# Kernel optimization log

Measured on AMD Instinct MI355X. Metric: run time of the kernel, lower is better.

## Reference

```python
import jax, jax.numpy as jnp
from jax import lax
import numpy as np

NEG = -1e9  # -inf surrogate for DP boundaries (matches deepblast's large-negative init)


def _lstm(xe, W_ih, W_hh, b):
    # xe: (B, T, D) -> hidden states (B, T, H). Single-layer LSTM via lax.scan.
    B, T, _ = xe.shape
    H = W_hh.shape[0]
    pre = xe @ W_ih + b  # precompute input contributions: (B, T, 4H)
    def step(carry, p):
        h, c = carry
        z = p + h @ W_hh
        i, f, g, o = jnp.split(z, 4, axis=-1)
        c = jax.nn.sigmoid(f) * c + jax.nn.sigmoid(i) * jnp.tanh(g)
        h = jax.nn.sigmoid(o) * jnp.tanh(c)
        return (h, c), h
    h0 = jnp.zeros((B, H), xe.dtype)
    _, hs = lax.scan(step, (h0, h0), jnp.swapaxes(pre, 0, 1))
    return jnp.swapaxes(hs, 0, 1)


def _embed(tok, emb, W_ih, W_hh, b_lstm, W_out, b_out):
    # StackedRNN: token embedding -> LSTM -> linear projection to nembed
    return _lstm(emb[tok], W_ih, W_hh, b_lstm) @ W_out + b_out


def _nw(theta, A):
    # Softmax-relaxed Needleman-Wunsch terminal value, anti-diagonal wavefront scan.
    # V[i,j] = theta[i-1,j-1] + logsumexp(V[i-1,j-1], V[i-1,j]+A, V[i,j-1]+A)
    B, N, M = theta.shape
    ii = jnp.arange(N + 1)
    d0 = jnp.full((B, N + 1), NEG, theta.dtype).at[:, 0].set(0.0)  # diag k=0: V[0,0]=0
    d1 = jnp.full((B, N + 1), NEG, theta.dtype)                    # diag k=1: boundaries
    def shift(a):  # a[i] -> a[i-1]
        return jnp.concatenate([jnp.full((a.shape[0], 1), NEG, a.dtype), a[:, :-1]], axis=1)
    def step(carry, k):
        p2, p1 = carry  # diagonals k-2, k-1; entry i holds V[i, (k-2)-i] / V[i, (k-1)-i]
        jj = k - ii
        valid = (ii >= 1) & (ii <= N) & (jj >= 1) & (jj <= M)
        td = theta[:, jnp.clip(ii - 1, 0, N - 1), jnp.clip(jj - 1, 0, M - 1)]  # (B, N+1)
        v = jax.nn.logsumexp(jnp.stack([shift(p1) + A, shift(p2), p1 + A], 0), axis=0)
        cur = jnp.where(valid[None, :], td + v, NEG)
        return (p1, cur), None
    (_, last), _ = lax.scan(step, (d0, d1), jnp.arange(2, N + M + 1))
    return last[:, N]  # V[N, M] per batch


def setup_inputs() -> dict:
    key = jax.random.key(0)
    ks = jax.random.split(key, 10)
    B, T, V, E, H = 32, 512, 22, 512, 512
    return {
        "x": jax.random.randint(ks[0], (B, T), 0, V),
        "y": jax.random.randint(ks[1], (B, T), 0, V),
        "emb": jax.random.normal(ks[2], (V, E), jnp.float32) * 0.1,
        "W_ih": jax.random.normal(ks[3], (E, 4 * H), jnp.float32) * 0.05,
        "W_hh": jax.random.normal(ks[4], (H, 4 * H), jnp.float32) * 0.05,
        "b_lstm": jnp.zeros((4 * H,), jnp.float32),
        "W_out": jax.random.normal(ks[5], (H, E), jnp.float32) * 0.05,
        "b_out": jnp.zeros((E,), jnp.float32),
        "W_gap": jax.random.normal(ks[6], (2 * E, 1), jnp.float32) * 0.05,
        "b_gap": jnp.zeros((1,), jnp.float32),
    }


def reference(x, y, emb, W_ih, W_hh, b_lstm, W_out, b_out, W_gap, b_gap):
    zx = _embed(x, emb, W_ih, W_hh, b_lstm, W_out, b_out)  # (B, N, E)
    zy = _embed(y, emb, W_ih, W_hh, b_lstm, W_out, b_out)  # (B, M, E)
    theta = jnp.einsum('bid,bjd->bij', zx, zy)             # (B, N, M)
    merged = jnp.concatenate([zx.mean(1), zy.mean(1)], axis=1)
    A = merged @ W_gap + b_gap                             # (B, 1) learned gap score
    return _nw(theta, A)                                   # (B,) DP terminal value
```

## Files before the change

kernel.cpp:

```cpp
#include <hip/hip_runtime.h>
#include <math.h>

#define TSEQ 512
#define HDIM 512
#define EDIM 512
#define NB   32
#define ROWS 64
#define GATES 2048
#define NEGV -1000000000.0f

typedef __attribute__((ext_vector_type(8))) short bf16x8;
typedef __attribute__((ext_vector_type(4))) float f32x4;

__device__ __forceinline__ float sigf(float x){ return 1.0f/(1.0f + __expf(-x)); }

__device__ __forceinline__ float tanhfast(float x){
  float t = __expf(-2.0f*fabsf(x));
  float r = (1.0f - t)/(1.0f + t);
  return copysignf(r, x);
}

__device__ __forceinline__ unsigned short f2bf(float f){
  unsigned int u = __builtin_bit_cast(unsigned int, f);
  unsigned int r = (u + 0x7fff + ((u>>16)&1)) >> 16;
  return (unsigned short)r;
}

__global__ __launch_bounds__(256) void table_k(const float* __restrict__ emb,
        const float* __restrict__ W_ih, const float* __restrict__ b_lstm,
        float* __restrict__ table){
  int j = blockIdx.x*256 + threadIdx.x;
  int v = blockIdx.y;
  float acc = b_lstm[j];
  #pragma unroll 4
  for(int k=0;k<EDIM;k++) acc = fmaf(emb[v*EDIM+k], W_ih[(size_t)k*GATES+j], acc);
  table[(size_t)v*GATES+j] = acc;
}

__global__ __launch_bounds__(64) void wprep_k(const float* __restrict__ W_hh,
        unsigned short* __restrict__ Wswz){
  int cid = blockIdx.x;
  int lane = threadIdx.x;
  int js = cid>>6, g = (cid>>4)&3, kc = cid&15;
  int col = g*512 + js*16 + (lane&15);
  int kbase = kc*32 + (lane>>4)*8;
  unsigned short v[8];
  #pragma unroll
  for(int e=0;e<8;e++) v[e] = f2bf(W_hh[(size_t)(kbase+e)*GATES + col]);
  *(uint4*)&Wswz[((size_t)cid*64 + lane)*8] = *(const uint4*)v;
}

__global__ __launch_bounds__(64) void wprep2_k(const float* __restrict__ W_out,
        unsigned short* __restrict__ wsw){
  int cid = blockIdx.x;
  int lane = threadIdx.x;
  int nc = cid>>4, kc = cid&15;
  int col = nc*16 + (lane&15);
  int kb = kc*32 + (lane>>4)*8;
  unsigned short v[8];
  #pragma unroll
  for(int e=0;e<8;e++) v[e] = f2bf(W_out[(size_t)(kb+e)*EDIM + col]);
  *(uint4*)&wsw[((size_t)cid*64 + lane)*8] = *(const uint4*)v;
}

__global__ __launch_bounds__(64,1) void lstm_wave(const int* __restrict__ x, const int* __restrict__ y,
        const float* __restrict__ table, const unsigned short* __restrict__ Wswz,
        unsigned* __restrict__ hx, unsigned short* __restrict__ hsb){
  __shared__ unsigned short wlds[32768];
  int w = blockIdx.x;
  int c = w>>6, mh = (w>>5)&1, js = w&31;
  int gid = w>>5;
  int lane = threadIdx.x;

  {
    const uint4* src = (const uint4*)(Wswz + (size_t)js*32768);
    uint4* dst = (uint4*)wlds;
    #pragma unroll
    for(int i=0;i<64;i++) dst[lane + i*64] = src[lane + i*64];
  }
  __syncthreads();

  const int* tokbase = c ? y : x;
  int jloc = lane&15;
  int j    = js*16 + jloc;
  int hi   = (j>>3)&3;
  int kc_o = j>>5;
  int e_o  = j&7;
  int rl0  = (lane>>4)*4;
  unsigned pub_vo = (unsigned)(((kc_o*64 + (rl0|(hi<<4)))*8 + e_o)*4);
  int rbase = c*32 + mh*16 + rl0;
  float cst[4] = {0.f,0.f,0.f,0.f};

  unsigned* gbase = hx + (size_t)gid*16384;
  unsigned vo32 = (unsigned)lane*32u;

  for(int s=0;s<TSEQ;s++){
    const unsigned* hin = gbase + (size_t)(s&1)*8192;
    unsigned* hout      = gbase + (size_t)((s+1)&1)*8192;
    unsigned tagexp = (unsigned)s;

    uint4 ra[32];
    while(true){
      #pragma unroll
      for(int kc=0;kc<16;kc++){
        asm volatile(
          "global_load_dwordx4 %0, %2, %3 sc0 sc1\n\t"
          "global_load_dwordx4 %1, %2, %3 offset:16 sc0 sc1"
          : "=&v"(ra[2*kc]), "=&v"(ra[2*kc+1])
          : "v"(vo32), "s"((const void*)(hin + (size_t)kc*512))
          : "memory");
      }
      asm volatile("s_waitcnt vmcnt(0)" ::: "memory");
      __builtin_amdgcn_sched_barrier(0);
      unsigned acc = 0u;
      #pragma unroll
      for(int i=0;i<32;i++)
        acc |= (ra[i].x ^ tagexp) | (ra[i].y ^ tagexp) | (ra[i].z ^ tagexp) | (ra[i].w ^ tagexp);
      if(__all((int)((acc & 0xFFFFu) == 0u))) break;
    }

    bf16x8 af[16];
    #pragma unroll
    for(int kc=0;kc<16;kc++){
      uint4 pk_;
      pk_.x = (ra[2*kc].x  >>16) | (ra[2*kc].y  & 0xFFFF0000u);
      pk_.y = (ra[2*kc].z  >>16) | (ra[2*kc].w  & 0xFFFF0000u);
      pk_.z = (ra[2*kc+1].x>>16) | (ra[2*kc+1].y& 0xFFFF0000u);
      pk_.w = (ra[2*kc+1].z>>16) | (ra[2*kc+1].w& 0xFFFF0000u);
      af[kc] = __builtin_bit_cast(bf16x8, pk_);
    }

    f32x4 acc0={0,0,0,0}, acc1={0,0,0,0}, acc2={0,0,0,0}, acc3={0,0,0,0};
    #pragma unroll
    for(int kc=0;kc<16;kc++){
      bf16x8 w0 = *(const bf16x8*)(const void*)&wlds[((0*16+kc)*64 + lane)*8];
      bf16x8 w1 = *(const bf16x8*)(const void*)&wlds[((1*16+kc)*64 + lane)*8];
      bf16x8 w2 = *(const bf16x8*)(const void*)&wlds[((2*16+kc)*64 + lane)*8];
      bf16x8 w3 = *(const bf16x8*)(const void*)&wlds[((3*16+kc)*64 + lane)*8];
      acc0 = __builtin_amdgcn_mfma_f32_16x16x32_bf16(af[kc], w0, acc0, 0,0,0);
      acc1 = __builtin_amdgcn_mfma_f32_16x16x32_bf16(af[kc], w1, acc1, 0,0,0);
      acc2 = __builtin_amdgcn_mfma_f32_16x16x32_bf16(af[kc], w2, acc2, 0,0,0);
      acc3 = __builtin_amdgcn_mfma_f32_16x16x32_bf16(af[kc], w3, acc3, 0,0,0);
    }

    unsigned hv[4]; unsigned short hb16[4];
    int sc = s>>4, sl = s&15;
    unsigned tagw = (unsigned)(s+1);
    #pragma unroll
    for(int q=0;q<4;q++){
      int tok = tokbase[(mh*16 + rl0 + q)*TSEQ + s];
      const float* tbl = table + (size_t)tok*GATES;
      float zi = acc0[q] + tbl[j];
      float zf = acc1[q] + tbl[512+j];
      float zg = acc2[q] + tbl[1024+j];
      float zo = acc3[q] + tbl[1536+j];
      float cn = sigf(zf)*cst[q] + sigf(zi)*tanhfast(zg);
      float h  = sigf(zo)*tanhfast(cn);
      cst[q] = cn;
      unsigned short hbv = f2bf(h);
      hb16[q] = hbv;
      hv[q] = ((unsigned)hbv<<16) | tagw;
    }
    asm volatile(
      "global_store_dword %[a], %[d0], %[sb] sc0 sc1\n\t"
      "global_store_dword %[a], %[d1], %[sb] offset:32 sc0 sc1\n\t"
      "global_store_dword %[a], %[d2], %[sb] offset:64 sc0 sc1\n\t"
      "global_store_dword %[a], %[d3], %[sb] offset:96 sc0 sc1"
      :: [a]"v"(pub_vo), [d0]"v"(hv[0]),[d1]"v"(hv[1]),[d2]"v"(hv[2]),[d3]"v"(hv[3]),
         [sb]"s"((void*)hout)
      : "memory");
    #pragma unroll
    for(int q=0;q<4;q++){
      int r = rbase + q;
      int mc = r*32 + sc;
      hsb[((size_t)(mc*16 + kc_o)*64 + (sl|(hi<<4)))*8 + e_o] = hb16[q];
    }
  }
}

__global__ __launch_bounds__(256) void zproj_mfma(const unsigned short* __restrict__ hsb,
        const unsigned short* __restrict__ woutswz, const float* __restrict__ b_out,
        float* __restrict__ z, unsigned short* __restrict__ zxA, unsigned short* __restrict__ zyB){
  int tid = threadIdx.x, wv = tid>>6, lane = tid&63;
  int m0 = blockIdx.x*128 + (wv>>1)*64;
  int n0 = blockIdx.y*128 + (wv&1)*64;
  int mc0 = m0>>4, nc0 = n0>>4;
  const uint4* ha = (const uint4*)hsb;
  const uint4* wb = (const uint4*)woutswz;
  f32x4 acc[4][4];
  #pragma unroll
  for(int i=0;i<4;i++)
    #pragma unroll
    for(int k2=0;k2<4;k2++) acc[i][k2] = (f32x4){0,0,0,0};
  for(int kc=0;kc<16;kc++){
    bf16x8 a[4], b[4];
    #pragma unroll
    for(int i=0;i<4;i++){
      a[i] = __builtin_bit_cast(bf16x8, ha[((size_t)((mc0+i)*16 + kc))*64 + lane]);
      b[i] = __builtin_bit_cast(bf16x8, wb[((size_t)((nc0+i)*16 + kc))*64 + lane]);
    }
    #pragma unroll
    for(int mi=0;mi<4;mi++)
      #pragma unroll
      for(int ci=0;ci<4;ci++)
        acc[mi][ci] = __builtin_amdgcn_mfma_f32_16x16x32_bf16(a[mi], b[ci], acc[mi][ci], 0,0,0);
  }
  int r = m0>>9;
  bool isx = (r < NB);
  unsigned short* zb = isx ? zxA : zyB;
  int bb = isx ? r : r-NB;
  #pragma unroll
  for(int ci=0;ci<4;ci++){
    int n = n0 + ci*16 + (lane&15);
    float bo = b_out[n];
    int kcz = n>>5, hi = (n>>3)&3, ez = n&7;
    #pragma unroll
    for(int mi=0;mi<4;mi++){
      #pragma unroll
      for(int q=0;q<4;q++){
        int m = m0 + mi*16 + (lane>>4)*4 + q;
        float zv = acc[mi][ci][q] + bo;
        z[(size_t)m*EDIM + n] = zv;
        int i = m&511;
        zb[(((size_t)(bb*32 + (i>>4))*16 + kcz)*64 + ((i&15)|(hi<<4)))*8 + ez] = f2bf(zv);
      }
    }
  }
}

__global__ __launch_bounds__(256) void theta_mfma(const unsigned short* __restrict__ zxA,
        const unsigned short* __restrict__ zyB, float* __restrict__ thetaD){
  int tid = threadIdx.x, wv = tid>>6, lane = tid&63;
  int b = blockIdx.z;
  int i0 = blockIdx.x*128 + (wv>>1)*64;
  int j0 = blockIdx.y*128 + (wv&1)*64;
  int ic0 = i0>>4, jc0 = j0>>4;
  const uint4* pa = (const uint4*)zxA;
  const uint4* pb = (const uint4*)zyB;
  f32x4 acc[4][4];
  #pragma unroll
  for(int i=0;i<4;i++)
    #pragma unroll
    for(int k2=0;k2<4;k2++) acc[i][k2] = (f32x4){0,0,0,0};
  for(int kc=0;kc<16;kc++){
    bf16x8 a[4], bfr[4];
    #pragma unroll
    for(int i=0;i<4;i++){
      a[i]   = __builtin_bit_cast(bf16x8, pa[((size_t)(b*32 + ic0+i)*16 + kc)*64 + lane]);
      bfr[i] = __builtin_bit_cast(bf16x8, pb[((size_t)(b*32 + jc0+i)*16 + kc)*64 + lane]);
    }
    #pragma unroll
    for(int mi=0;mi<4;mi++)
      #pragma unroll
      for(int ci=0;ci<4;ci++)
        acc[mi][ci] = __builtin_amdgcn_mfma_f32_16x16x32_bf16(a[mi], bfr[ci], acc[mi][ci], 0,0,0);
  }
  #pragma unroll
  for(int mi=0;mi<4;mi++){
    #pragma unroll
    for(int ci=0;ci<4;ci++){
      #pragma unroll
      for(int q=0;q<4;q++){
        int i  = i0 + mi*16 + (lane>>4)*4 + q;
        int jj = j0 + ci*16 + (lane&15);
        thetaD[((size_t)b*1023 + (i+jj))*512 + i] = acc[mi][ci][q];
      }
    }
  }
}

__global__ __launch_bounds__(256) void mean_k(const float* __restrict__ z, float* __restrict__ zmean){
  int r = blockIdx.x;
  int tid = threadIdx.x;
  for(int ee=tid; ee<EDIM; ee+=256){
    float acc=0.f;
    for(int t=0;t<TSEQ;t++) acc += z[((size_t)r*TSEQ+t)*EDIM+ee];
    zmean[(size_t)r*EDIM+ee] = acc*(1.0f/TSEQ);
  }
}

__global__ __launch_bounds__(256) void gap_k(const float* __restrict__ zmean,
        const float* __restrict__ W_gap, const float* __restrict__ b_gap, float* __restrict__ Aout){
  __shared__ float red[256];
  int b = blockIdx.x;
  int tid = threadIdx.x;
  float acc=0.f;
  for(int i=tid;i<2*EDIM;i+=256){
    float m = (i<EDIM)? zmean[(size_t)b*EDIM+i] : zmean[(size_t)(b+NB)*EDIM + (i-EDIM)];
    acc = fmaf(m, W_gap[i], acc);
  }
  red[tid]=acc; __syncthreads();
  for(int s=128;s>0;s>>=1){ if(tid<s) red[tid]+=red[tid+s]; __syncthreads(); }
  if(tid==0) Aout[b] = red[0] + b_gap[0];
}

__global__ __launch_bounds__(64) void nw_k(const float* __restrict__ thetaD,
        const float* __restrict__ Aout, float* __restrict__ out){
  const float L2E = 1.4426950408889634f, LN2 = 0.6931471805599453f;
  int b = blockIdx.x;
  int lane = threadIdx.x;
  float A = Aout[b];
  const float* thD = thetaD + (size_t)b*1023*512;
  float p1[8], p2[8];
  #pragma unroll
  for(int i=0;i<8;i++){ p1[i]=NEGV; p2[i]=NEGV; }
  float p1_0 = NEGV, p2_0 = 0.0f;
  float4 ta = *(const float4*)&thD[(size_t)lane*8];
  float4 tb = *(const float4*)&thD[(size_t)lane*8+4];
  for(int k=2;k<=1024;k++){
    float4 na, nb;
    if(k<1024){
      na = *(const float4*)&thD[(size_t)(k-1)*512 + lane*8];
      nb = *(const float4*)&thD[(size_t)(k-1)*512 + lane*8+4];
    }
    float pm1 = __shfl_up(p1[7],1);
    float pm2 = __shfl_up(p2[7],1);
    if(lane==0){ pm1 = p1_0; pm2 = p2_0; }
    float td[8] = {ta.x,ta.y,ta.z,ta.w,tb.x,tb.y,tb.z,tb.w};
    float cur[8];
    #pragma unroll
    for(int cx=0;cx<8;cx++){
      int i = lane*8+1+cx;
      int jq = k-i;
      bool valid = (jq>=1)&&(jq<=512);
      float a  = (cx==0? pm1 : p1[cx-1]) + A;
      float bb = (cx==0? pm2 : p2[cx-1]);
      float cc = p1[cx] + A;
      float m = fmaxf(fmaxf(a,bb),cc);
      float sum = exp2f((a-m)*L2E) + exp2f((bb-m)*L2E) + exp2f((cc-m)*L2E);
      float v = m + log2f(sum)*LN2;
      cur[cx] = valid ? td[cx] + v : NEGV;
    }
    #pragma unroll
    for(int cx=0;cx<8;cx++){ p2[cx]=p1[cx]; p1[cx]=cur[cx]; }
    p2_0 = p1_0; p1_0 = NEGV;
    ta = na; tb = nb;
  }
  if(lane==63) out[b] = p1[7];
}

extern "C" void kernel_launch(void* const* d_in, const int* in_sizes, int n_in,
                              void* d_out, int out_size, void* d_ws, size_t ws_size,
                              hipStream_t stream) {
  (void)in_sizes; (void)n_in; (void)out_size; (void)ws_size;
  const int*   x      = (const int*)d_in[0];
  const int*   y      = (const int*)d_in[1];
  const float* emb    = (const float*)d_in[2];
  const float* W_ih   = (const float*)d_in[3];
  const float* W_hh   = (const float*)d_in[4];
  const float* b_lstm = (const float*)d_in[5];
  const float* W_out  = (const float*)d_in[6];
  const float* b_out  = (const float*)d_in[7];
  const float* W_gap  = (const float*)d_in[8];
  const float* b_gap  = (const float*)d_in[9];
  float* out = (float*)d_out;

  char* ws = (char*)d_ws;
  const size_t OFF_TABLE = 0;
  const size_t OFF_WSWZ  = 184320;
  const size_t OFF_WOUT  = OFF_WSWZ  + 2097152;
  const size_t OFF_HX    = OFF_WOUT  + 524288;
  const size_t OFF_HSB   = OFF_HX    + 262144;
  const size_t OFF_Z     = OFF_HSB   + 33554432;
  const size_t OFF_ZXA   = OFF_Z     + 67108864;
  const size_t OFF_ZYB   = OFF_ZXA   + 16777216;
  const size_t OFF_THD   = OFF_ZYB   + 16777216;
  const size_t OFF_ZMEAN = OFF_THD   + 67043328;
  const size_t OFF_AOUT  = OFF_ZMEAN + 131072;
  float* table = (float*)(ws + OFF_TABLE);
  unsigned short* Wswz    = (unsigned short*)(ws + OFF_WSWZ);
  unsigned short* woutswz = (unsigned short*)(ws + OFF_WOUT);
  unsigned* hx = (unsigned*)(ws + OFF_HX);
  unsigned short* hsb = (unsigned short*)(ws + OFF_HSB);
  float* z     = (float*)(ws + OFF_Z);
  unsigned short* zxA = (unsigned short*)(ws + OFF_ZXA);
  unsigned short* zyB = (unsigned short*)(ws + OFF_ZYB);
  float* thetaD = (float*)(ws + OFF_THD);
  float* zmean = (float*)(ws + OFF_ZMEAN);
  float* Aout  = (float*)(ws + OFF_AOUT);

  hipMemsetAsync(hx, 0, 262144, stream);

  table_k<<<dim3(8,22), 256, 0, stream>>>(emb, W_ih, b_lstm, table);
  wprep_k<<<2048, 64, 0, stream>>>(W_hh, Wswz);
  wprep2_k<<<512, 64, 0, stream>>>(W_out, woutswz);
  lstm_wave<<<128, 64, 0, stream>>>(x, y, table, Wswz, hx, hsb);
  zproj_mfma<<<dim3(256,4), 256, 0, stream>>>(hsb, woutswz, b_out, z, zxA, zyB);
  theta_mfma<<<dim3(4,4,32), 256, 0, stream>>>(zxA, zyB, thetaD);
  mean_k<<<64, 256, 0, stream>>>(z, zmean);
  gap_k<<<32, 256, 0, stream>>>(zmean, W_gap, b_gap, Aout);
  nw_k<<<32, 64, 0, stream>>>(thetaD, Aout, out);
}
```

Before: 3.013 ms.

## Register-resident LSTM weights, fused mean, bf16 theta with tiled diagonal transpose

Several changes at once. The LSTM kernel keeps three of the four gate weight slices in registers and only the fourth in LDS, prefetches the token table values before the spin-wait, adds s_sleep to the poll loop, and swaps divisions for rcp. The projection kernel stops writing the full fp32 z and instead accumulates column sums into zmean with atomics, which removes the mean kernel. Theta is stored in bf16 row-major and a new LDS-tiled kernel reorders it to anti-diagonal layout, replacing the earlier scattered writes; the NW kernel reads bf16. This cuts memory traffic and per-step latency, at the cost of bf16 precision in theta, heavy register pressure, and possibly extra latency from the sleep.

```diff
diff --git a/kernel.cpp b/kernel.cpp
--- a/kernel.cpp
+++ b/kernel.cpp
@@ -12,11 +12,11 @@
 typedef __attribute__((ext_vector_type(8))) short bf16x8;
 typedef __attribute__((ext_vector_type(4))) float f32x4;
 
-__device__ __forceinline__ float sigf(float x){ return 1.0f/(1.0f + __expf(-x)); }
+__device__ __forceinline__ float sigf(float x){ return __builtin_amdgcn_rcpf(1.0f + __expf(-x)); }
 
 __device__ __forceinline__ float tanhfast(float x){
   float t = __expf(-2.0f*fabsf(x));
-  float r = (1.0f - t)/(1.0f + t);
+  float r = (1.0f - t)*__builtin_amdgcn_rcpf(1.0f + t);
   return copysignf(r, x);
 }
 
@@ -24,6 +24,11 @@
   unsigned int u = __builtin_bit_cast(unsigned int, f);
   unsigned int r = (u + 0x7fff + ((u>>16)&1)) >> 16;
   return (unsigned short)r;
+}
+
+__device__ __forceinline__ float bf2f(unsigned short v){
+  unsigned int u = ((unsigned int)v)<<16;
+  return __builtin_bit_cast(float, u);
 }
 
 __global__ __launch_bounds__(256) void table_k(const float* __restrict__ emb,
@@ -66,17 +71,26 @@
 __global__ __launch_bounds__(64,1) void lstm_wave(const int* __restrict__ x, const int* __restrict__ y,
         const float* __restrict__ table, const unsigned short* __restrict__ Wswz,
         unsigned* __restrict__ hx, unsigned short* __restrict__ hsb){
-  __shared__ unsigned short wlds[32768];
+  __shared__ unsigned short wlds[8192];
   int w = blockIdx.x;
   int c = w>>6, mh = (w>>5)&1, js = w&31;
-  int gid = w>>5;
+  int gid = c*2 + mh;
   int lane = threadIdx.x;
 
+  bf16x8 wf[48];
   {
-    const uint4* src = (const uint4*)(Wswz + (size_t)js*32768);
+    const unsigned short* wp = Wswz + (size_t)js*32768;
+    #pragma unroll
+    for(int g=0;g<3;g++)
+      #pragma unroll
+      for(int kc=0;kc<16;kc++)
+        wf[g*16+kc] = *(const bf16x8*)(const void*)&wp[((size_t)(g*16+kc)*64 + lane)*8];
+  }
+  {
+    const uint4* src = (const uint4*)(Wswz + (size_t)js*32768 + 48*512);
     uint4* dst = (uint4*)wlds;
     #pragma unroll
-    for(int i=0;i<64;i++) dst[lane + i*64] = src[lane + i*64];
+    for(int i=0;i<16;i++) dst[lane + i*64] = src[lane + i*64];
   }
   __syncthreads();
 
@@ -99,7 +113,20 @@
     unsigned* hout      = gbase + (size_t)((s+1)&1)*8192;
     unsigned tagexp = (unsigned)s;
 
+    float tb[4][4];
+    {
+      int toks[4];
+      #pragma unroll
+      for(int q=0;q<4;q++) toks[q] = tokbase[(mh*16 + rl0 + q)*TSEQ + s];
+      #pragma unroll
+      for(int q=0;q<4;q++){
+        const float* tbl = table + (size_t)toks[q]*GATES;
+        tb[0][q]=tbl[j]; tb[1][q]=tbl[512+j]; tb[2][q]=tbl[1024+j]; tb[3][q]=tbl[1536+j];
+      }
+    }
+
     uint4 ra[32];
+    int att = 0;
     while(true){
       #pragma unroll
       for(int kc=0;kc<16;kc++){
@@ -117,9 +144,11 @@
       for(int i=0;i<32;i++)
         acc |= (ra[i].x ^ tagexp) | (ra[i].y ^ tagexp) | (ra[i].z ^ tagexp) | (ra[i].w ^ tagexp);
       if(__all((int)((acc & 0xFFFFu) == 0u))) break;
-    }
-
-    bf16x8 af[16];
+      __builtin_amdgcn_s_sleep(2);
+      att++;
+    }
+
+    f32x4 acc0={0,0,0,0}, acc1={0,0,0,0}, acc2={0,0,0,0}, acc3={0,0,0,0};
     #pragma unroll
     for(int kc=0;kc<16;kc++){
       uint4 pk_;
@@ -127,20 +156,12 @@
       pk_.y = (ra[2*kc].z  >>16) | (ra[2*kc].w  & 0xFFFF0000u);
       pk_.z = (ra[2*kc+1].x>>16) | (ra[2*kc+1].y& 0xFFFF0000u);
       pk_.w = (ra[2*kc+1].z>>16) | (ra[2*kc+1].w& 0xFFFF0000u);
-      af[kc] = __builtin_bit_cast(bf16x8, pk_);
-    }
-
-    f32x4 acc0={0,0,0,0}, acc1={0,0,0,0}, acc2={0,0,0,0}, acc3={0,0,0,0};
-    #pragma unroll
-    for(int kc=0;kc<16;kc++){
-      bf16x8 w0 = *(const bf16x8*)(const void*)&wlds[((0*16+kc)*64 + lane)*8];
-      bf16x8 w1 = *(const bf16x8*)(const void*)&wlds[((1*16+kc)*64 + lane)*8];
-      bf16x8 w2 = *(const bf16x8*)(const void*)&wlds[((2*16+kc)*64 + lane)*8];
-      bf16x8 w3 = *(const bf16x8*)(const void*)&wlds[((3*16+kc)*64 + lane)*8];
-      acc0 = __builtin_amdgcn_mfma_f32_16x16x32_bf16(af[kc], w0, acc0, 0,0,0);
-      acc1 = __builtin_amdgcn_mfma_f32_16x16x32_bf16(af[kc], w1, acc1, 0,0,0);
-      acc2 = __builtin_amdgcn_mfma_f32_16x16x32_bf16(af[kc], w2, acc2, 0,0,0);
-      acc3 = __builtin_amdgcn_mfma_f32_16x16x32_bf16(af[kc], w3, acc3, 0,0,0);
+      bf16x8 afk = __builtin_bit_cast(bf16x8, pk_);
+      acc0 = __builtin_amdgcn_mfma_f32_16x16x32_bf16(afk, wf[kc],    acc0, 0,0,0);
+      acc1 = __builtin_amdgcn_mfma_f32_16x16x32_bf16(afk, wf[16+kc], acc1, 0,0,0);
+      acc2 = __builtin_amdgcn_mfma_f32_16x16x32_bf16(afk, wf[32+kc], acc2, 0,0,0);
+      bf16x8 b3 = *(const bf16x8*)(const void*)&wlds[((size_t)kc*64 + lane)*8];
+      acc3 = __builtin_amdgcn_mfma_f32_16x16x32_bf16(afk, b3,        acc3, 0,0,0);
     }
 
     unsigned hv[4]; unsigned short hb16[4];
@@ -148,12 +169,10 @@
     unsigned tagw = (unsigned)(s+1);
     #pragma unroll
     for(int q=0;q<4;q++){
-      int tok = tokbase[(mh*16 + rl0 + q)*TSEQ + s];
-      const float* tbl = table + (size_t)tok*GATES;
-      float zi = acc0[q] + tbl[j];
-      float zf = acc1[q] + tbl[512+j];
-      float zg = acc2[q] + tbl[1024+j];
-      float zo = acc3[q] + tbl[1536+j];
+      float zi = acc0[q] + tb[0][q];
+      float zf = acc1[q] + tb[1][q];
+      float zg = acc2[q] + tb[2][q];
+      float zo = acc3[q] + tb[3][q];
       float cn = sigf(zf)*cst[q] + sigf(zi)*tanhfast(zg);
       float h  = sigf(zo)*tanhfast(cn);
       cst[q] = cn;
@@ -180,7 +199,8 @@
 
 __global__ __launch_bounds__(256) void zproj_mfma(const unsigned short* __restrict__ hsb,
         const unsigned short* __restrict__ woutswz, const float* __restrict__ b_out,
-        float* __restrict__ z, unsigned short* __restrict__ zxA, unsigned short* __restrict__ zyB){
+        unsigned short* __restrict__ zxA, unsigned short* __restrict__ zyB,
+        float* __restrict__ zmean){
   int tid = threadIdx.x, wv = tid>>6, lane = tid&63;
   int m0 = blockIdx.x*128 + (wv>>1)*64;
   int n0 = blockIdx.y*128 + (wv&1)*64;
@@ -214,22 +234,26 @@
     int n = n0 + ci*16 + (lane&15);
     float bo = b_out[n];
     int kcz = n>>5, hi = (n>>3)&3, ez = n&7;
+    float colsum = 0.f;
     #pragma unroll
     for(int mi=0;mi<4;mi++){
       #pragma unroll
       for(int q=0;q<4;q++){
         int m = m0 + mi*16 + (lane>>4)*4 + q;
         float zv = acc[mi][ci][q] + bo;
-        z[(size_t)m*EDIM + n] = zv;
+        colsum += acc[mi][ci][q];
         int i = m&511;
         zb[(((size_t)(bb*32 + (i>>4))*16 + kcz)*64 + ((i&15)|(hi<<4)))*8 + ez] = f2bf(zv);
       }
     }
+    colsum += __shfl_xor(colsum, 16);
+    colsum += __shfl_xor(colsum, 32);
+    if((lane>>4)==0) atomicAdd(&zmean[(size_t)r*EDIM + n], colsum);
   }
 }
 
 __global__ __launch_bounds__(256) void theta_mfma(const unsigned short* __restrict__ zxA,
-        const unsigned short* __restrict__ zyB, float* __restrict__ thetaD){
+        const unsigned short* __restrict__ zyB, unsigned short* __restrict__ th_n){
   int tid = threadIdx.x, wv = tid>>6, lane = tid&63;
   int b = blockIdx.z;
   int i0 = blockIdx.x*128 + (wv>>1)*64;
@@ -263,30 +287,53 @@
       for(int q=0;q<4;q++){
         int i  = i0 + mi*16 + (lane>>4)*4 + q;
         int jj = j0 + ci*16 + (lane&15);
-        thetaD[((size_t)b*1023 + (i+jj))*512 + i] = acc[mi][ci][q];
+        th_n[((size_t)b*TSEQ + i)*TSEQ + jj] = f2bf(acc[mi][ci][q]);
       }
     }
   }
 }
 
-__global__ __launch_bounds__(256) void mean_k(const float* __restrict__ z, float* __restrict__ zmean){
-  int r = blockIdx.x;
+#define DP 136
+__global__ __launch_bounds__(128) void diag_k(const unsigned short* __restrict__ th_n,
+        unsigned short* __restrict__ thD){
+  __shared__ unsigned short t[128*DP];
+  int b = blockIdx.z;
+  int i0 = blockIdx.x*128;
+  int j0 = blockIdx.y*128;
   int tid = threadIdx.x;
-  for(int ee=tid; ee<EDIM; ee+=256){
-    float acc=0.f;
-    for(int t=0;t<TSEQ;t++) acc += z[((size_t)r*TSEQ+t)*EDIM+ee];
-    zmean[(size_t)r*EDIM+ee] = acc*(1.0f/TSEQ);
+  {
+    int cc = (tid&7)*16;
+    for(int rr = tid>>3; rr<128; rr+=16){
+      const uint4* src = (const uint4*)&th_n[((size_t)(b*TSEQ + i0+rr))*TSEQ + j0 + cc];
+      uint4 v0 = src[0], v1 = src[1];
+      *(uint4*)&t[rr*DP + cc]     = v0;
+      *(uint4*)&t[rr*DP + cc + 8] = v1;
+    }
+  }
+  __syncthreads();
+  for(int u=0;u<255;u++){
+    int d = i0 + j0 + u;
+    int ibeg = (u>127) ? (d - j0 - 127) : i0;
+    int iend = (u<128) ? (d - j0)       : (i0+127);
+    int len = iend - ibeg + 1;
+    if(tid < len){
+      int i = ibeg + tid;
+      thD[((size_t)b*1023 + d)*TSEQ + i] = t[(i-i0)*DP + (d-i-j0)];
+    }
   }
 }
 
 __global__ __launch_bounds__(256) void gap_k(const float* __restrict__ zmean,
-        const float* __restrict__ W_gap, const float* __restrict__ b_gap, float* __restrict__ Aout){
+        const float* __restrict__ b_out, const float* __restrict__ W_gap,
+        const float* __restrict__ b_gap, float* __restrict__ Aout){
   __shared__ float red[256];
   int b = blockIdx.x;
   int tid = threadIdx.x;
   float acc=0.f;
   for(int i=tid;i<2*EDIM;i+=256){
-    float m = (i<EDIM)? zmean[(size_t)b*EDIM+i] : zmean[(size_t)(b+NB)*EDIM + (i-EDIM)];
+    int e = (i<EDIM)? i : i-EDIM;
+    float msum = (i<EDIM)? zmean[(size_t)b*EDIM+e] : zmean[(size_t)(b+NB)*EDIM+e];
+    float m = msum*(1.0f/TSEQ) + b_out[e];
     acc = fmaf(m, W_gap[i], acc);
   }
   red[tid]=acc; __syncthreads();
@@ -294,29 +341,29 @@
   if(tid==0) Aout[b] = red[0] + b_gap[0];
 }
 
-__global__ __launch_bounds__(64) void nw_k(const float* __restrict__ thetaD,
+__global__ __launch_bounds__(64) void nw_k(const unsigned short* __restrict__ thD,
         const float* __restrict__ Aout, float* __restrict__ out){
   const float L2E = 1.4426950408889634f, LN2 = 0.6931471805599453f;
   int b = blockIdx.x;
   int lane = threadIdx.x;
   float A = Aout[b];
-  const float* thD = thetaD + (size_t)b*1023*512;
+  const unsigned short* thb = thD + (size_t)b*1023*TSEQ;
   float p1[8], p2[8];
   #pragma unroll
   for(int i=0;i<8;i++){ p1[i]=NEGV; p2[i]=NEGV; }
   float p1_0 = NEGV, p2_0 = 0.0f;
-  float4 ta = *(const float4*)&thD[(size_t)lane*8];
-  float4 tb = *(const float4*)&thD[(size_t)lane*8+4];
+  uint4 ta = *(const uint4*)&thb[(size_t)lane*8];
   for(int k=2;k<=1024;k++){
-    float4 na, nb;
-    if(k<1024){
-      na = *(const float4*)&thD[(size_t)(k-1)*512 + lane*8];
-      nb = *(const float4*)&thD[(size_t)(k-1)*512 + lane*8+4];
-    }
+    uint4 na = ta;
+    if(k<1024) na = *(const uint4*)&thb[(size_t)(k-1)*TSEQ + lane*8];
+    float td[8];
+    td[0]=bf2f((unsigned short)(ta.x&0xFFFF)); td[1]=bf2f((unsigned short)(ta.x>>16));
+    td[2]=bf2f((unsigned short)(ta.y&0xFFFF)); td[3]=bf2f((unsigned short)(ta.y>>16));
+    td[4]=bf2f((unsigned short)(ta.z&0xFFFF)); td[5]=bf2f((unsigned short)(ta.z>>16));
+    td[6]=bf2f((unsigned short)(ta.w&0xFFFF)); td[7]=bf2f((unsigned short)(ta.w>>16));
     float pm1 = __shfl_up(p1[7],1);
     float pm2 = __shfl_up(p2[7],1);
     if(lane==0){ pm1 = p1_0; pm2 = p2_0; }
-    float td[8] = {ta.x,ta.y,ta.z,ta.w,tb.x,tb.y,tb.z,tb.w};
     float cur[8];
     #pragma unroll
     for(int cx=0;cx<8;cx++){
@@ -334,7 +381,7 @@
     #pragma unroll
     for(int cx=0;cx<8;cx++){ p2[cx]=p1[cx]; p1[cx]=cur[cx]; }
     p2_0 = p1_0; p1_0 = NEGV;
-    ta = na; tb = nb;
+    ta = na;
   }
   if(lane==63) out[b] = p1[7];
 }
@@ -361,33 +408,34 @@
   const size_t OFF_WOUT  = OFF_WSWZ  + 2097152;
   const size_t OFF_HX    = OFF_WOUT  + 524288;
   const size_t OFF_HSB   = OFF_HX    + 262144;
-  const size_t OFF_Z     = OFF_HSB   + 33554432;
-  const size_t OFF_ZXA   = OFF_Z     + 67108864;
+  const size_t OFF_ZXA   = OFF_HSB   + 33554432;
   const size_t OFF_ZYB   = OFF_ZXA   + 16777216;
-  const size_t OFF_THD   = OFF_ZYB   + 16777216;
-  const size_t OFF_ZMEAN = OFF_THD   + 67043328;
+  const size_t OFF_THN   = OFF_ZYB   + 16777216;
+  const size_t OFF_THD   = OFF_THN   + 33554432;
+  const size_t OFF_ZMEAN = OFF_THD   + 33521664;
   const size_t OFF_AOUT  = OFF_ZMEAN + 131072;
   float* table = (float*)(ws + OFF_TABLE);
   unsigned short* Wswz    = (unsigned short*)(ws + OFF_WSWZ);
   unsigned short* woutswz = (unsigned short*)(ws + OFF_WOUT);
   unsigned* hx = (unsigned*)(ws + OFF_HX);
-  unsigned short* hsb = (unsigned short*)(ws + OFF_HSB);
-  float* z     = (float*)(ws + OFF_Z);
-  unsigned short* zxA = (unsigned short*)(ws + OFF_ZXA);
-  unsigned short* zyB = (unsigned short*)(ws + OFF_ZYB);
-  float* thetaD = (float*)(ws + OFF_THD);
+  unsigned short* hsb  = (unsigned short*)(ws + OFF_HSB);
+  unsigned short* zxA  = (unsigned short*)(ws + OFF_ZXA);
+  unsigned short* zyB  = (unsigned short*)(ws + OFF_ZYB);
+  unsigned short* th_n = (unsigned short*)(ws + OFF_THN);
+  unsigned short* thD  = (unsigned short*)(ws + OFF_THD);
   float* zmean = (float*)(ws + OFF_ZMEAN);
   float* Aout  = (float*)(ws + OFF_AOUT);
 
   hipMemsetAsync(hx, 0, 262144, stream);
+  hipMemsetAsync(zmean, 0, 131072, stream);
 
   table_k<<<dim3(8,22), 256, 0, stream>>>(emb, W_ih, b_lstm, table);
   wprep_k<<<2048, 64, 0, stream>>>(W_hh, Wswz);
   wprep2_k<<<512, 64, 0, stream>>>(W_out, woutswz);
   lstm_wave<<<128, 64, 0, stream>>>(x, y, table, Wswz, hx, hsb);
-  zproj_mfma<<<dim3(256,4), 256, 0, stream>>>(hsb, woutswz, b_out, z, zxA, zyB);
-  theta_mfma<<<dim3(4,4,32), 256, 0, stream>>>(zxA, zyB, thetaD);
-  mean_k<<<64, 256, 0, stream>>>(z, zmean);
-  gap_k<<<32, 256, 0, stream>>>(zmean, W_gap, b_gap, Aout);
-  nw_k<<<32, 64, 0, stream>>>(thetaD, Aout, out);
-}
+  zproj_mfma<<<dim3(256,4), 256, 0, stream>>>(hsb, woutswz, b_out, zxA, zyB, zmean);
+  theta_mfma<<<dim3(4,4,32), 256, 0, stream>>>(zxA, zyB, th_n);
+  diag_k<<<dim3(4,4,32), 128, 0, stream>>>(th_n, thD);
+  gap_k<<<32, 256, 0, stream>>>(zmean, b_out, W_gap, b_gap, Aout);
+  nw_k<<<32, 64, 0, stream>>>(thD, Aout, out);
+}
```

After: 2.634 ms. 12.6% less time.
